# Performance work log

Hardware: AMD Instinct MI355X
Metric: run time of the kernel (lower is better)

## Reference

```python
import jax, jax.numpy as jnp
import numpy as np

N_NODES, N_EDGES, N_GRAPHS = 50000, 800000, 64
F_NODE, F_EDGE, F_GLOB, F_MSG, F_OUT, HID = 64, 64, 64, 64, 128, 32


def setup_inputs() -> dict:
    key = jax.random.key(0)
    ks = jax.random.split(key, 16)
    s = lambda fan_in: 1.0 / np.sqrt(fan_in)
    inp = {
        "x": jax.random.normal(ks[0], (N_NODES, F_NODE), dtype=jnp.float32),
        "edge_index": jax.random.randint(ks[1], (2, N_EDGES), 0, N_NODES),
        "edge_attr": jax.random.normal(ks[2], (N_EDGES, F_EDGE), dtype=jnp.float32),
        "u": jax.random.normal(ks[3], (N_GRAPHS, F_GLOB), dtype=jnp.float32),
        "batch": jnp.sort(jax.random.randint(ks[4], (N_NODES,), 0, N_GRAPHS)),
        # node_mlp_1: Lin(2*F_NODE+F_EDGE, 32) -> ReLU -> Lin(32, F_MSG) -> ReLU
        "W1": jax.random.normal(ks[5], (2 * F_NODE + F_EDGE, HID), dtype=jnp.float32) * s(2 * F_NODE + F_EDGE),
        "b1": jnp.zeros((HID,), jnp.float32),
        "W2": jax.random.normal(ks[6], (HID, F_MSG), dtype=jnp.float32) * s(HID),
        "b2": jnp.zeros((F_MSG,), jnp.float32),
        # node_mlp_2: Lin(2*F_MSG+F_NODE+F_GLOB, 32) -> ReLU -> Lin(32, F_OUT) -> ReLU
        "W3": jax.random.normal(ks[7], (2 * F_MSG + F_NODE + F_GLOB, HID), dtype=jnp.float32) * s(2 * F_MSG + F_NODE + F_GLOB),
        "b3": jnp.zeros((HID,), jnp.float32),
        "W4": jax.random.normal(ks[8], (HID, F_OUT), dtype=jnp.float32) * s(HID),
        "b4": jnp.zeros((F_OUT,), jnp.float32),
    }
    return inp


def reference(x, edge_index, edge_attr, u, batch, W1, b1, W2, b2, W3, b3, W4, b4):
    N = x.shape[0]
    row, col = edge_index[0], edge_index[1]
    # edge MLP (dropout off / eval mode)
    m = jnp.concatenate([x[row], x[col], edge_attr], axis=1)  # [E, 2F+Fe]
    m = jax.nn.relu(m @ W1 + b1)
    m = jax.nn.relu(m @ W2 + b2)  # [E, F_MSG]
    # scatter-mean and scatter-max onto destination nodes (col)
    cnt = jax.ops.segment_sum(jnp.ones((col.shape[0], 1), m.dtype), col, num_segments=N)  # [N,1]
    agg_mean = jax.ops.segment_sum(m, col, num_segments=N) / jnp.maximum(cnt, 1.0)
    agg_max = jax.ops.segment_max(m, col, num_segments=N)
    agg_max = jnp.where(cnt > 0, agg_max, 0.0)  # empty segments -> 0 (torch_scatter convention)
    # node MLP
    h = jnp.concatenate([x, agg_mean, agg_max, u[batch]], axis=1)
    h = jax.nn.relu(h @ W3 + b3)
    return jax.nn.relu(h @ W4 + b4)
```

## Files before the change

### kernel.cpp

```cpp
#include <hip/hip_runtime.h>
#include <hip/hip_bf16.h>
#include <stdint.h>

constexpr int FN   = 64;
constexpr int HIDN = 32;
constexpr int FMSG = 64;
constexpr int FOUT = 128;

using short8 = __attribute__((ext_vector_type(8))) short;
using f32x4  = __attribute__((ext_vector_type(4))) float;

union Frag { short8 v; uint32_t u[4]; };

__device__ __forceinline__ uint32_t packrn(float a, float b) {
    union { __hip_bfloat162 h; uint32_t u; } cv;
    cv.h = __float22bfloat162_rn(make_float2(a, b));
    return cv.u;
}
__device__ __forceinline__ float bf16_to_f(uint32_t h16) {
    return __uint_as_float(h16 << 16);
}

__device__ __forceinline__ int node_of(const int* __restrict__ offs, int N, int target) {
    int l = 0, r = N + 1;
    while (l + 1 < r) {
        const int m = (l + r) >> 1;
        if (offs[m] <= target) l = m; else r = m;
    }
    return l;
}

__global__ __launch_bounds__(256) void zero_cnt_kernel(int* __restrict__ cnt, int N)
{
    const int i = blockIdx.x * 256 + threadIdx.x;
    if (i < N) cnt[i] = 0;
}

__global__ __launch_bounds__(256) void hist_kernel(
    const int* __restrict__ ei, int* __restrict__ cnt, int* __restrict__ rank,
    int E)
{
    const int e4 = (blockIdx.x * 256 + threadIdx.x) * 4;
    if (e4 + 3 < E) {
        const int4 c = *reinterpret_cast<const int4*>(ei + E + e4);
        int4 r;
        r.x = atomicAdd(cnt + c.x, 1);
        r.y = atomicAdd(cnt + c.y, 1);
        r.z = atomicAdd(cnt + c.z, 1);
        r.w = atomicAdd(cnt + c.w, 1);
        *reinterpret_cast<int4*>(rank + e4) = r;
    } else {
        for (int e = e4; e < E; ++e) rank[e] = atomicAdd(cnt + ei[E + e], 1);
    }
}

__global__ __launch_bounds__(256) void prep_rest_kernel(
    const float* __restrict__ x, const float* __restrict__ u,
    const float* __restrict__ W1, const float* __restrict__ b1,
    const float* __restrict__ W2,
    const float* __restrict__ W3, const float* __restrict__ b3,
    const float* __restrict__ W4,
    float* __restrict__ Pa, float* __restrict__ Pb, float* __restrict__ Qc,
    float* __restrict__ Qu,
    uint32_t* __restrict__ PW1, uint32_t* __restrict__ PW2,
    uint32_t* __restrict__ PW3, uint32_t* __restrict__ PW4,
    uint4* __restrict__ zbase, size_t zquads,
    int N, int G, int BP, int BZ)
{
    const int b   = blockIdx.x;
    const int tid = threadIdx.x;

    if (b < BP) {
        const int n = b * 256 + tid;
        if (n >= N) return;
        float a[HIDN], bq[HIDN], c[HIDN];
#pragma unroll
        for (int j = 0; j < HIDN; ++j) { a[j] = b1[j]; bq[j] = 0.0f; c[j] = b3[j]; }
        const float* xr = x + (size_t)n * FN;
        const float* WA = W1;
        const float* WB = W1 + FN * HIDN;
        const float* WX = W3;
#pragma unroll 2
        for (int k = 0; k < FN; k += 4) {
            const float4 v = *reinterpret_cast<const float4*>(xr + k);
            const float* wa = WA + k * HIDN;
            const float* wb = WB + k * HIDN;
            const float* wc = WX + k * HIDN;
#pragma unroll
            for (int j = 0; j < HIDN; ++j) {
                float aj = a[j], bj = bq[j], cj = c[j];
                aj = fmaf(v.x, wa[j], aj);            bj = fmaf(v.x, wb[j], bj);            cj = fmaf(v.x, wc[j], cj);
                aj = fmaf(v.y, wa[HIDN + j], aj);     bj = fmaf(v.y, wb[HIDN + j], bj);     cj = fmaf(v.y, wc[HIDN + j], cj);
                aj = fmaf(v.z, wa[2 * HIDN + j], aj); bj = fmaf(v.z, wb[2 * HIDN + j], bj); cj = fmaf(v.z, wc[2 * HIDN + j], cj);
                aj = fmaf(v.w, wa[3 * HIDN + j], aj); bj = fmaf(v.w, wb[3 * HIDN + j], bj); cj = fmaf(v.w, wc[3 * HIDN + j], cj);
                a[j] = aj; bq[j] = bj; c[j] = cj;
            }
        }
        float4* pa = reinterpret_cast<float4*>(Pa + (size_t)n * HIDN);
        float4* pb = reinterpret_cast<float4*>(Pb + (size_t)n * HIDN);
        float4* qc = reinterpret_cast<float4*>(Qc + (size_t)n * HIDN);
#pragma unroll
        for (int q = 0; q < HIDN / 4; ++q) {
            pa[q] = make_float4(a[4*q], a[4*q+1], a[4*q+2], a[4*q+3]);
            pb[q] = make_float4(bq[4*q], bq[4*q+1], bq[4*q+2], bq[4*q+3]);
            qc[q] = make_float4(c[4*q], c[4*q+1], c[4*q+2], c[4*q+3]);
        }
        return;
    }
    if (b == BP) {
        const float* WC = W1 + 2 * FN * HIDN;
        for (int i = tid; i < 1024; i += 256) {
            const int j = i >> 5, k2 = i & 31;
            PW1[i] = packrn(WC[(2 * k2) * HIDN + j], WC[(2 * k2 + 1) * HIDN + j]);
        }
        for (int i = tid; i < 1024; i += 256) {
            const int j = i >> 4, k2 = i & 15;
            PW2[i] = packrn(W2[(2 * k2) * FMSG + j], W2[(2 * k2 + 1) * FMSG + j]);
        }
        const float* W3m = W3 + 64 * HIDN;
        for (int i = tid; i < 2048; i += 256) {
            const int j = i >> 6, k2 = i & 63;
            PW3[i] = packrn(W3m[(2 * k2) * HIDN + j], W3m[(2 * k2 + 1) * HIDN + j]);
        }
        for (int i = tid; i < 2048; i += 256) {
            const int j = i >> 4, k2 = i & 15;
            PW4[i] = packrn(W4[(2 * k2) * FOUT + j], W4[(2 * k2 + 1) * FOUT + j]);
        }
        const float* W3u = W3 + 192 * HIDN;
        for (int i = tid; i < G * HIDN; i += 256) {
            const int g = i >> 5, j = i & 31;
            const float* ur = u + (size_t)g * FN;
            float acc = 0.0f;
#pragma unroll 8
            for (int k = 0; k < FN; ++k) acc = fmaf(ur[k], W3u[k * HIDN + j], acc);
            Qu[i] = acc;
        }
        return;
    }
    const size_t stride = (size_t)BZ * 256;
    const uint4 z = make_uint4(0u, 0u, 0u, 0u);
    for (size_t i = (size_t)(b - BP - 1) * 256 + tid; i < zquads; i += stride)
        zbase[i] = z;
}

__global__ __launch_bounds__(256) void scanA_kernel(
    const int* __restrict__ cnt, int* __restrict__ part, int N)
{
    __shared__ int red[256];
    const int tid  = threadIdx.x;
    const int base = blockIdx.x * 2048 + tid * 8;
    int s = 0;
    if (base + 8 <= N) {
        const int4 a = *reinterpret_cast<const int4*>(cnt + base);
        const int4 b = *reinterpret_cast<const int4*>(cnt + base + 4);
        s = a.x + a.y + a.z + a.w + b.x + b.y + b.z + b.w;
    } else {
        for (int i = base; i < min(base + 8, N); ++i) s += cnt[i];
    }
    red[tid] = s;
    __syncthreads();
    for (int d = 128; d > 0; d >>= 1) {
        if (tid < d) red[tid] += red[tid + d];
        __syncthreads();
    }
    if (tid == 0) part[blockIdx.x] = red[0];
}

__global__ __launch_bounds__(64) void scanB_kernel(
    const int* __restrict__ part, int* __restrict__ partx,
    int* __restrict__ offs, int NB, int N)
{
    if (threadIdx.x == 0) {
        int run = 0;
        for (int i = 0; i < NB; ++i) { partx[i] = run; run += part[i]; }
        offs[N] = run;
    }
}

__global__ __launch_bounds__(256) void scanC_kernel(
    const int* __restrict__ cnt, const int* __restrict__ partx,
    int* __restrict__ offs, int N)
{
    __shared__ int sb[256];
    const int tid  = threadIdx.x;
    const int base = blockIdx.x * 2048 + tid * 8;
    int v[8];
    int tsum = 0;
#pragma unroll
    for (int q = 0; q < 8; ++q) {
        const int i = base + q;
        v[q] = (i < N) ? cnt[i] : 0;
        tsum += v[q];
    }
    sb[tid] = tsum;
    __syncthreads();
    for (int d = 1; d < 256; d <<= 1) {
        const int t = (tid >= d) ? sb[tid - d] : 0;
        __syncthreads();
        sb[tid] += t;
        __syncthreads();
    }
    int run = partx[blockIdx.x] + sb[tid] - tsum;
#pragma unroll
    for (int q = 0; q < 8; ++q) {
        const int i = base + q;
        if (i < N) offs[i] = run;
        run += v[q];
    }
}

__global__ __launch_bounds__(256) void scatter_ntile_kernel(
    const int* __restrict__ ei, const int* __restrict__ offs,
    const int* __restrict__ rank, int4* __restrict__ re4,
    int2* __restrict__ ntile, int E, int N, int NT, int SB)
{
    const int tid = threadIdx.x;
    if ((int)blockIdx.x < SB) {
        const int e = blockIdx.x * 256 + tid;
        if (e >= E) return;
        const int row = ei[e];
        const int col = ei[E + e];
        const int pos = offs[col] + rank[e];
        re4[pos] = make_int4(row, col, e, 0);
    } else {
        const int t = ((int)blockIdx.x - SB) * 256 + tid;
        if (t >= NT) return;
        const int a = node_of(offs, N, t * 64);
        const int b = node_of(offs, N, min(t * 64 + 63, E - 1));
        ntile[t] = make_int2(a, b);
    }
}

__global__ __launch_bounds__(128) void fused_edge_mfma(
    const float* __restrict__ ea,
    const uint32_t* __restrict__ PW1, const uint32_t* __restrict__ PW2,
    const float* __restrict__ b2,
    const float* __restrict__ Pa, const float* __restrict__ Pb,
    const int4* __restrict__ re4, const int* __restrict__ offs,
    const int2* __restrict__ ntile,
    float* __restrict__ agg_sum, int* __restrict__ agg_maxb,
    int N, int E, int NT)
{
    __shared__ uint32_t smem_all[2 * 64 * 34];
    const int w    = threadIdx.x >> 6;
    const int t    = blockIdx.x * 2 + w;
    if (t >= NT) return;
    uint32_t* smem = smem_all + w * (64 * 34);
    const int lane = threadIdx.x & 63;
    const int l15  = lane & 15;
    const int l4   = lane >> 4;
    const int e0   = t * 64;
    const int e1   = min(e0 + 64, E);
    const int2 nrange = ntile[t];

    const int p = e0 + lane;
    const int4 rce = re4[min(p, E - 1)];
    {
        const float2* pa = reinterpret_cast<const float2*>(Pa + (size_t)rce.x * HIDN);
        const float2* pb = reinterpret_cast<const float2*>(Pb + (size_t)rce.y * HIDN);
        float2* dst = reinterpret_cast<float2*>(&smem[lane * 34]);
#pragma unroll
        for (int q = 0; q < 16; ++q) {
            const float2 a = pa[q], b = pb[q];
            dst[q] = make_float2(a.x + b.x, a.y + b.y);
        }
    }

    Frag B1[2][2];
#pragma unroll
    for (int nt = 0; nt < 2; ++nt)
#pragma unroll
        for (int ks = 0; ks < 2; ++ks) {
            const uint4 q = *reinterpret_cast<const uint4*>(
                &PW1[(nt * 16 + l15) * 32 + ks * 16 + l4 * 4]);
            B1[nt][ks].u[0] = q.x; B1[nt][ks].u[1] = q.y;
            B1[nt][ks].u[2] = q.z; B1[nt][ks].u[3] = q.w;
        }
    Frag B2f[4];
#pragma unroll
    for (int nt = 0; nt < 4; ++nt) {
        const uint4 q = *reinterpret_cast<const uint4*>(
            &PW2[(nt * 16 + l15) * 16 + l4 * 4]);
        B2f[nt].u[0] = q.x; B2f[nt].u[1] = q.y;
        B2f[nt].u[2] = q.z; B2f[nt].u[3] = q.w;
    }

    Frag A1[4][2];
#pragma unroll
    for (int mt = 0; mt < 4; ++mt) {
        const int eix = __shfl(rce.z, mt * 16 + l15, 64);
        const float* rp = ea + (size_t)eix * FN;
#pragma unroll
        for (int ks = 0; ks < 2; ++ks) {
            const float4* gp = reinterpret_cast<const float4*>(rp + ks * 32 + l4 * 8);
            const float4 f0 = gp[0], f1 = gp[1];
            A1[mt][ks].u[0] = packrn(f0.x, f0.y);
            A1[mt][ks].u[1] = packrn(f0.z, f0.w);
            A1[mt][ks].u[2] = packrn(f1.x, f1.y);
            A1[mt][ks].u[3] = packrn(f1.z, f1.w);
        }
    }

    f32x4 acc1[4][2];
    const float* Pl = reinterpret_cast<const float*>(smem);
#pragma unroll
    for (int mt = 0; mt < 4; ++mt)
#pragma unroll
        for (int nt = 0; nt < 2; ++nt)
#pragma unroll
            for (int r = 0; r < 4; ++r) {
                const int et = mt * 16 + l4 * 4 + r;
                acc1[mt][nt][r] = Pl[et * 34 + nt * 16 + l15];
            }
#pragma unroll
    for (int mt = 0; mt < 4; ++mt)
#pragma unroll
        for (int nt = 0; nt < 2; ++nt)
#pragma unroll
            for (int ks = 0; ks < 2; ++ks)
                acc1[mt][nt] = __builtin_amdgcn_mfma_f32_16x16x32_bf16(
                    A1[mt][ks].v, B1[nt][ks].v, acc1[mt][nt], 0, 0, 0);

    float* Hl = reinterpret_cast<float*>(smem);
#pragma unroll
    for (int mt = 0; mt < 4; ++mt)
#pragma unroll
        for (int nt = 0; nt < 2; ++nt)
#pragma unroll
            for (int r = 0; r < 4; ++r) {
                const int et = mt * 16 + l4 * 4 + r;
                Hl[et * 34 + nt * 16 + l15] = fmaxf(acc1[mt][nt][r], 0.0f);
            }

    Frag A2[4];
#pragma unroll
    for (int mt = 0; mt < 4; ++mt) {
        const float* hb = &Hl[(mt * 16 + l15) * 34 + l4 * 8];
        const float2 g0 = *reinterpret_cast<const float2*>(hb + 0);
        const float2 g1 = *reinterpret_cast<const float2*>(hb + 2);
        const float2 g2 = *reinterpret_cast<const float2*>(hb + 4);
        const float2 g3 = *reinterpret_cast<const float2*>(hb + 6);
        A2[mt].u[0] = packrn(g0.x, g0.y);
        A2[mt].u[1] = packrn(g1.x, g1.y);
        A2[mt].u[2] = packrn(g2.x, g2.y);
        A2[mt].u[3] = packrn(g3.x, g3.y);
    }

#pragma unroll
    for (int nt = 0; nt < 4; ++nt) {
        const float b2v = b2[nt * 16 + l15];
        f32x4 a2c[4];
#pragma unroll
        for (int mt = 0; mt < 4; ++mt) {
            a2c[mt] = (f32x4){0.f, 0.f, 0.f, 0.f};
            a2c[mt] = __builtin_amdgcn_mfma_f32_16x16x32_bf16(
                A2[mt].v, B2f[nt].v, a2c[mt], 0, 0, 0);
        }
        const int j = nt * 16 + l15;
#pragma unroll
        for (int mt = 0; mt < 4; ++mt)
#pragma unroll
            for (int rp2 = 0; rp2 < 2; ++rp2) {
                const int q2 = mt * 8 + l4 * 2 + rp2;
                const float v0 = fmaxf(a2c[mt][rp2 * 2]     + b2v, 0.0f);
                const float v1 = fmaxf(a2c[mt][rp2 * 2 + 1] + b2v, 0.0f);
                smem[q2 * 64 + (j ^ (((q2 >> 1) & 1) << 4))] = packrn(v0, v1);
            }
    }

    const int n0 = nrange.x, n1 = nrange.y;
    for (int n = n0; n <= n1; ++n) {
        const int s0 = offs[n], t0 = offs[n + 1];
        const int sl = max(s0, e0) - e0, tl = min(t0, e1) - e0;
        float sum = 0.0f, mx = 0.0f;
        int q = sl;
        if (q < tl && (q & 1)) {
            const int q2 = q >> 1;
            const uint32_t wv = smem[q2 * 64 + (lane ^ (((q2 >> 1) & 1) << 4))];
            const float v = bf16_to_f(wv >> 16);
            sum += v; mx = fmaxf(mx, v); ++q;
        }
        for (; q + 1 < tl; q += 2) {
            const int q2 = q >> 1;
            const uint32_t wv = smem[q2 * 64 + (lane ^ (((q2 >> 1) & 1) << 4))];
            const float v0 = bf16_to_f(wv & 0xffffu), v1 = bf16_to_f(wv >> 16);
            sum += v0 + v1; mx = fmaxf(mx, fmaxf(v0, v1));
        }
        if (q < tl) {
            const int q2 = q >> 1;
            const uint32_t wv = smem[q2 * 64 + (lane ^ (((q2 >> 1) & 1) << 4))];
            const float v = bf16_to_f(wv & 0xffffu);
            sum += v; mx = fmaxf(mx, v);
        }
        float* sp = agg_sum  + (size_t)n * FMSG + lane;
        int*   mp = agg_maxb + (size_t)n * FMSG + lane;
        if (s0 >= e0 && t0 <= e1) {
            *sp = sum;
            *mp = __float_as_int(mx);
        } else {
            unsafeAtomicAdd(sp, sum);
            atomicMax(mp, __float_as_int(mx));
        }
    }
}

__global__ __launch_bounds__(256) void node_mfma(
    const float* __restrict__ Qc, const float* __restrict__ Qu,
    const int*   __restrict__ batch,
    const uint32_t* __restrict__ PW3, const uint32_t* __restrict__ PW4,
    const float* __restrict__ b4,
    const float* __restrict__ agg_sum, const int* __restrict__ agg_maxb,
    const int*   __restrict__ offs,
    float* __restrict__ out, int N)
{
    __shared__ float Hl_all[4 * 32 * 34];
    const int w    = threadIdx.x >> 6;
    float* Hl      = Hl_all + w * (32 * 34);
    const int lane = threadIdx.x & 63;
    const int l15  = lane & 15;
    const int l4   = lane >> 4;
    const int n0   = blockIdx.x * 128 + w * 32;
    if (n0 >= N) return;

    f32x4 acc1[2][2];
#pragma unroll
    for (int mt = 0; mt < 2; ++mt)
#pragma unroll
        for (int r = 0; r < 4; ++r) {
            const int nc = min(n0 + mt * 16 + l4 * 4 + r, N - 1);
            const int g  = batch[nc];
#pragma unroll
            for (int nt = 0; nt < 2; ++nt)
                acc1[mt][nt][r] = Qc[(size_t)nc * HIDN + nt * 16 + l15]
                                + Qu[(size_t)g  * HIDN + nt * 16 + l15];
        }

    int   arn[2];
    float ainv[2];
#pragma unroll
    for (int mt = 0; mt < 2; ++mt) {
        arn[mt] = min(n0 + mt * 16 + l15, N - 1);
        const int deg = offs[arn[mt] + 1] - offs[arn[mt]];
        ainv[mt] = (deg > 0) ? 1.0f / (float)deg : 0.0f;
    }

    Frag B3[2][4];
#pragma unroll
    for (int nt = 0; nt < 2; ++nt)
#pragma unroll
        for (int ks = 0; ks < 4; ++ks) {
            const uint4 q = *reinterpret_cast<const uint4*>(
                &PW3[(nt * 16 + l15) * 64 + ks * 16 + l4 * 4]);
            B3[nt][ks].u[0] = q.x; B3[nt][ks].u[1] = q.y;
            B3[nt][ks].u[2] = q.z; B3[nt][ks].u[3] = q.w;
        }

#pragma unroll
    for (int ks = 0; ks < 4; ++ks) {
        Frag A[2];
        if (ks < 2) {
#pragma unroll
            for (int mt = 0; mt < 2; ++mt) {
                const float4* gp = reinterpret_cast<const float4*>(
                    agg_sum + (size_t)arn[mt] * FMSG + ks * 32 + l4 * 8);
                const float4 f0 = gp[0], f1 = gp[1];
                const float s = ainv[mt];
                A[mt].u[0] = packrn(f0.x * s, f0.y * s);
                A[mt].u[1] = packrn(f0.z * s, f0.w * s);
                A[mt].u[2] = packrn(f1.x * s, f1.y * s);
                A[mt].u[3] = packrn(f1.z * s, f1.w * s);
            }
        } else {
#pragma unroll
            for (int mt = 0; mt < 2; ++mt) {
                const uint4* gp = reinterpret_cast<const uint4*>(
                    agg_maxb + (size_t)arn[mt] * FMSG + (ks - 2) * 32 + l4 * 8);
                const uint4 u0 = gp[0], u1 = gp[1];
                A[mt].u[0] = packrn(__uint_as_float(u0.x), __uint_as_float(u0.y));
                A[mt].u[1] = packrn(__uint_as_float(u0.z), __uint_as_float(u0.w));
                A[mt].u[2] = packrn(__uint_as_float(u1.x), __uint_as_float(u1.y));
                A[mt].u[3] = packrn(__uint_as_float(u1.z), __uint_as_float(u1.w));
            }
        }
#pragma unroll
        for (int mt = 0; mt < 2; ++mt)
#pragma unroll
            for (int nt = 0; nt < 2; ++nt)
                acc1[mt][nt] = __builtin_amdgcn_mfma_f32_16x16x32_bf16(
                    A[mt].v, B3[nt][ks].v, acc1[mt][nt], 0, 0, 0);
    }

#pragma unroll
    for (int mt = 0; mt < 2; ++mt)
#pragma unroll
        for (int nt = 0; nt < 2; ++nt)
#pragma unroll
            for (int r = 0; r < 4; ++r) {
                const int rw = mt * 16 + l4 * 4 + r;
                Hl[rw * 34 + nt * 16 + l15] = fmaxf(acc1[mt][nt][r], 0.0f);
            }

    Frag A2[2];
#pragma unroll
    for (int mt = 0; mt < 2; ++mt) {
        const float* hb = &Hl[(mt * 16 + l15) * 34 + l4 * 8];
        const float2 g0 = *reinterpret_cast<const float2*>(hb + 0);
        const float2 g1 = *reinterpret_cast<const float2*>(hb + 2);
        const float2 g2 = *reinterpret_cast<const float2*>(hb + 4);
        const float2 g3 = *reinterpret_cast<const float2*>(hb + 6);
        A2[mt].u[0] = packrn(g0.x, g0.y);
        A2[mt].u[1] = packrn(g1.x, g1.y);
        A2[mt].u[2] = packrn(g2.x, g2.y);
        A2[mt].u[3] = packrn(g3.x, g3.y);
    }

#pragma unroll
    for (int nt = 0; nt < 8; ++nt) {
        Frag B4f;
        const uint4 q = *reinterpret_cast<const uint4*>(
            &PW4[(nt * 16 + l15) * 16 + l4 * 4]);
        B4f.u[0] = q.x; B4f.u[1] = q.y; B4f.u[2] = q.z; B4f.u[3] = q.w;
        const float b4v = b4[nt * 16 + l15];
        f32x4 tacc[2];
#pragma unroll
        for (int mt = 0; mt < 2; ++mt) {
            tacc[mt] = (f32x4){0.f, 0.f, 0.f, 0.f};
            tacc[mt] = __builtin_amdgcn_mfma_f32_16x16x32_bf16(
                A2[mt].v, B4f.v, tacc[mt], 0, 0, 0);
        }
#pragma unroll
        for (int mt = 0; mt < 2; ++mt)
#pragma unroll
            for (int r = 0; r < 4; ++r) {
                const int node = n0 + mt * 16 + l4 * 4 + r;
                if (node < N)
                    out[(size_t)node * FOUT + nt * 16 + l15] =
                        fmaxf(tacc[mt][r] + b4v, 0.0f);
            }
    }
}

extern "C" void kernel_launch(void* const* d_in, const int* in_sizes, int n_in,
                              void* d_out, int out_size, void* d_ws, size_t ws_size,
                              hipStream_t stream)
{
    const float* x     = (const float*)d_in[0];
    const int*   ei    = (const int*)  d_in[1];
    const float* ea    = (const float*)d_in[2];
    const float* u     = (const float*)d_in[3];
    const int*   batch = (const int*)  d_in[4];
    const float* W1    = (const float*)d_in[5];
    const float* b1    = (const float*)d_in[6];
    const float* W2    = (const float*)d_in[7];
    const float* b2    = (const float*)d_in[8];
    const float* W3    = (const float*)d_in[9];
    const float* b3    = (const float*)d_in[10];
    const float* W4    = (const float*)d_in[11];
    const float* b4    = (const float*)d_in[12];
    float* out = (float*)d_out;

    const int N = in_sizes[0] / FN;
    const int E = in_sizes[1] / 2;
    const int G = in_sizes[3] / FN;
    const int NT = (E + 63) / 64;

    char* wp = (char*)d_ws;
    auto take = [&](size_t bytes) -> void* {
        void* r = (void*)wp;
        wp += (bytes + 255) & ~(size_t)255;
        return r;
    };
    float*    agg_sum  = (float*)   take((size_t)N * FMSG * 4);
    int*      agg_maxb = (int*)     take((size_t)N * FMSG * 4);
    char*     zero_end = wp;
    int*      cnt      = (int*)     take((size_t)N * 4);
    int*      offs     = (int*)     take(((size_t)N + 1) * 4);
    int*      rank     = (int*)     take((size_t)E * 4);
    int4*     re4      = (int4*)    take((size_t)E * 16);
    int2*     ntile    = (int2*)    take((size_t)NT * 8);
    float*    Pa       = (float*)   take((size_t)N * HIDN * 4);
    float*    Pb       = (float*)   take((size_t)N * HIDN * 4);
    float*    Qc       = (float*)   take((size_t)N * HIDN * 4);
    float*    Qu       = (float*)   take((size_t)G * HIDN * 4);
    uint32_t* PW1      = (uint32_t*)take(1024 * 4);
    uint32_t* PW2      = (uint32_t*)take(1024 * 4);
    uint32_t* PW3      = (uint32_t*)take(2048 * 4);
    uint32_t* PW4      = (uint32_t*)take(2048 * 4);
    int*      part     = (int*)     take(64 * 4);
    int*      partx    = (int*)     take(64 * 4);

    const int BH = (E / 4 + 255) / 256;
    const int BP = (N + 255) / 256;
    const int BZ = 256;
    const int NB = (N + 2047) / 2048;
    const int SB = (E + 255) / 256;
    const int TB = (NT + 255) / 256;
    const size_t zquads = (size_t)(zero_end - (char*)agg_sum) / 16;

    zero_cnt_kernel<<<(N + 255) / 256, 256, 0, stream>>>(cnt, N);
    hist_kernel   <<<BH, 256, 0, stream>>>(ei, cnt, rank, E);
    prep_rest_kernel<<<BP + 1 + BZ, 256, 0, stream>>>(
        x, u, W1, b1, W2, W3, b3, W4,
        Pa, Pb, Qc, Qu, PW1, PW2, PW3, PW4,
        (uint4*)agg_sum, zquads, N, G, BP, BZ);
    scanA_kernel  <<<NB, 256, 0, stream>>>(cnt, part, N);
    scanB_kernel  <<<1, 64, 0, stream>>>(part, partx, offs, NB, N);
    scanC_kernel  <<<NB, 256, 0, stream>>>(cnt, partx, offs, N);
    scatter_ntile_kernel<<<SB + TB, 256, 0, stream>>>(
        ei, offs, rank, re4, ntile, E, N, NT, SB);
    fused_edge_mfma<<<(NT + 1) / 2, 128, 0, stream>>>(
        ea, PW1, PW2, b2, Pa, Pb, re4, offs, ntile, agg_sum, agg_maxb, N, E, NT);
    node_mfma     <<<(N + 127) / 128, 256, 0, stream>>>(
        Qc, Qu, batch, PW3, PW4, b4, agg_sum, agg_maxb, offs, out, N);
}
```

Before: 226.5 us.

## Split node precompute into LDS-staged kernel and simplify histogram to one edge per thread

The per-node projection (x·W1a, x·W1b, x·W3x) moves into its own kernel. Each wave first stages 64 rows of x into padded shared memory with coalesced float4 loads, instead of every thread reading its own row with strided accesses. The weight packing, Qu and zeroing work move to a separate tail kernel. The histogram kernel now handles one edge per thread rather than four via int4, which trades memory-level parallelism per thread for more threads. The change adds a kernel launch and cuts the per-block thread count of the node kernel to 128.

```diff
diff --git a/kernel.cpp b/kernel.cpp
--- a/kernel.cpp
+++ b/kernel.cpp
@@ -40,74 +40,85 @@
     const int* __restrict__ ei, int* __restrict__ cnt, int* __restrict__ rank,
     int E)
 {
-    const int e4 = (blockIdx.x * 256 + threadIdx.x) * 4;
-    if (e4 + 3 < E) {
-        const int4 c = *reinterpret_cast<const int4*>(ei + E + e4);
-        int4 r;
-        r.x = atomicAdd(cnt + c.x, 1);
-        r.y = atomicAdd(cnt + c.y, 1);
-        r.z = atomicAdd(cnt + c.z, 1);
-        r.w = atomicAdd(cnt + c.w, 1);
-        *reinterpret_cast<int4*>(rank + e4) = r;
-    } else {
-        for (int e = e4; e < E; ++e) rank[e] = atomicAdd(cnt + ei[E + e], 1);
-    }
-}
-
-__global__ __launch_bounds__(256) void prep_rest_kernel(
-    const float* __restrict__ x, const float* __restrict__ u,
+    const int e = blockIdx.x * 256 + threadIdx.x;
+    if (e < E) rank[e] = atomicAdd(cnt + ei[E + e], 1);
+}
+
+__global__ __launch_bounds__(128) void node_pre_kernel(
+    const float* __restrict__ x,
     const float* __restrict__ W1, const float* __restrict__ b1,
-    const float* __restrict__ W2,
     const float* __restrict__ W3, const float* __restrict__ b3,
-    const float* __restrict__ W4,
     float* __restrict__ Pa, float* __restrict__ Pb, float* __restrict__ Qc,
+    int N)
+{
+    __shared__ float xs_all[2 * 64 * 65];
+    const int w    = threadIdx.x >> 6;
+    const int lane = threadIdx.x & 63;
+    float* xs = xs_all + w * (64 * 65);
+    const int nbase = blockIdx.x * 128 + w * 64;
+    if (nbase >= N) return;
+
+#pragma unroll
+    for (int j = 0; j < 16; ++j) {
+        const int idx = j * 64 + lane;
+        const int row = idx >> 4, cq = idx & 15;
+        const int nr  = min(nbase + row, N - 1);
+        const float4 v = *reinterpret_cast<const float4*>(x + (size_t)nr * FN + cq * 4);
+        float* d = xs + row * 65 + cq * 4;
+        d[0] = v.x; d[1] = v.y; d[2] = v.z; d[3] = v.w;
+    }
+
+    const int n = nbase + lane;
+    if (n >= N) return;
+
+    float a[HIDN], bq[HIDN], c[HIDN];
+#pragma unroll
+    for (int j = 0; j < HIDN; ++j) { a[j] = b1[j]; bq[j] = 0.0f; c[j] = b3[j]; }
+    const float* xr = xs + lane * 65;
+    const float* WA = W1;
+    const float* WB = W1 + FN * HIDN;
+    const float* WX = W3;
+#pragma unroll 2
+    for (int k = 0; k < FN; k += 4) {
+        const float v0 = xr[k], v1 = xr[k + 1], v2 = xr[k + 2], v3 = xr[k + 3];
+        const float* wa = WA + k * HIDN;
+        const float* wb = WB + k * HIDN;
+        const float* wc = WX + k * HIDN;
+#pragma unroll
+        for (int j = 0; j < HIDN; ++j) {
+            float aj = a[j], bj = bq[j], cj = c[j];
+            aj = fmaf(v0, wa[j], aj);            bj = fmaf(v0, wb[j], bj);            cj = fmaf(v0, wc[j], cj);
+            aj = fmaf(v1, wa[HIDN + j], aj);     bj = fmaf(v1, wb[HIDN + j], bj);     cj = fmaf(v1, wc[HIDN + j], cj);
+            aj = fmaf(v2, wa[2 * HIDN + j], aj); bj = fmaf(v2, wb[2 * HIDN + j], bj); cj = fmaf(v2, wc[2 * HIDN + j], cj);
+            aj = fmaf(v3, wa[3 * HIDN + j], aj); bj = fmaf(v3, wb[3 * HIDN + j], bj); cj = fmaf(v3, wc[3 * HIDN + j], cj);
+            a[j] = aj; bq[j] = bj; c[j] = cj;
+        }
+    }
+    float4* pa = reinterpret_cast<float4*>(Pa + (size_t)n * HIDN);
+    float4* pb = reinterpret_cast<float4*>(Pb + (size_t)n * HIDN);
+    float4* qc = reinterpret_cast<float4*>(Qc + (size_t)n * HIDN);
+#pragma unroll
+    for (int q = 0; q < HIDN / 4; ++q) {
+        pa[q] = make_float4(a[4*q], a[4*q+1], a[4*q+2], a[4*q+3]);
+        pb[q] = make_float4(bq[4*q], bq[4*q+1], bq[4*q+2], bq[4*q+3]);
+        qc[q] = make_float4(c[4*q], c[4*q+1], c[4*q+2], c[4*q+3]);
+    }
+}
+
+__global__ __launch_bounds__(256) void prep_tail_kernel(
+    const float* __restrict__ u,
+    const float* __restrict__ W1, const float* __restrict__ W2,
+    const float* __restrict__ W3, const float* __restrict__ W4,
     float* __restrict__ Qu,
     uint32_t* __restrict__ PW1, uint32_t* __restrict__ PW2,
     uint32_t* __restrict__ PW3, uint32_t* __restrict__ PW4,
     uint4* __restrict__ zbase, size_t zquads,
-    int N, int G, int BP, int BZ)
+    int G, int BZ)
 {
     const int b   = blockIdx.x;
     const int tid = threadIdx.x;
 
-    if (b < BP) {
-        const int n = b * 256 + tid;
-        if (n >= N) return;
-        float a[HIDN], bq[HIDN], c[HIDN];
-#pragma unroll
-        for (int j = 0; j < HIDN; ++j) { a[j] = b1[j]; bq[j] = 0.0f; c[j] = b3[j]; }
-        const float* xr = x + (size_t)n * FN;
-        const float* WA = W1;
-        const float* WB = W1 + FN * HIDN;
-        const float* WX = W3;
-#pragma unroll 2
-        for (int k = 0; k < FN; k += 4) {
-            const float4 v = *reinterpret_cast<const float4*>(xr + k);
-            const float* wa = WA + k * HIDN;
-            const float* wb = WB + k * HIDN;
-            const float* wc = WX + k * HIDN;
-#pragma unroll
-            for (int j = 0; j < HIDN; ++j) {
-                float aj = a[j], bj = bq[j], cj = c[j];
-                aj = fmaf(v.x, wa[j], aj);            bj = fmaf(v.x, wb[j], bj);            cj = fmaf(v.x, wc[j], cj);
-                aj = fmaf(v.y, wa[HIDN + j], aj);     bj = fmaf(v.y, wb[HIDN + j], bj);     cj = fmaf(v.y, wc[HIDN + j], cj);
-                aj = fmaf(v.z, wa[2 * HIDN + j], aj); bj = fmaf(v.z, wb[2 * HIDN + j], bj); cj = fmaf(v.z, wc[2 * HIDN + j], cj);
-                aj = fmaf(v.w, wa[3 * HIDN + j], aj); bj = fmaf(v.w, wb[3 * HIDN + j], bj); cj = fmaf(v.w, wc[3 * HIDN + j], cj);
-                a[j] = aj; bq[j] = bj; c[j] = cj;
-            }
-        }
-        float4* pa = reinterpret_cast<float4*>(Pa + (size_t)n * HIDN);
-        float4* pb = reinterpret_cast<float4*>(Pb + (size_t)n * HIDN);
-        float4* qc = reinterpret_cast<float4*>(Qc + (size_t)n * HIDN);
-#pragma unroll
-        for (int q = 0; q < HIDN / 4; ++q) {
-            pa[q] = make_float4(a[4*q], a[4*q+1], a[4*q+2], a[4*q+3]);
-            pb[q] = make_float4(bq[4*q], bq[4*q+1], bq[4*q+2], bq[4*q+3]);
-            qc[q] = make_float4(c[4*q], c[4*q+1], c[4*q+2], c[4*q+3]);
-        }
-        return;
-    }
-    if (b == BP) {
+    if (b == 0) {
         const float* WC = W1 + 2 * FN * HIDN;
         for (int i = tid; i < 1024; i += 256) {
             const int j = i >> 5, k2 = i & 31;
@@ -139,7 +150,7 @@
     }
     const size_t stride = (size_t)BZ * 256;
     const uint4 z = make_uint4(0u, 0u, 0u, 0u);
-    for (size_t i = (size_t)(b - BP - 1) * 256 + tid; i < zquads; i += stride)
+    for (size_t i = (size_t)(b - 1) * 256 + tid; i < zquads; i += stride)
         zbase[i] = z;
 }
 
@@ -589,8 +600,6 @@
     int*      part     = (int*)     take(64 * 4);
     int*      partx    = (int*)     take(64 * 4);
 
-    const int BH = (E / 4 + 255) / 256;
-    const int BP = (N + 255) / 256;
     const int BZ = 256;
     const int NB = (N + 2047) / 2048;
     const int SB = (E + 255) / 256;
@@ -598,18 +607,19 @@
     const size_t zquads = (size_t)(zero_end - (char*)agg_sum) / 16;
 
     zero_cnt_kernel<<<(N + 255) / 256, 256, 0, stream>>>(cnt, N);
-    hist_kernel   <<<BH, 256, 0, stream>>>(ei, cnt, rank, E);
-    prep_rest_kernel<<<BP + 1 + BZ, 256, 0, stream>>>(
-        x, u, W1, b1, W2, W3, b3, W4,
-        Pa, Pb, Qc, Qu, PW1, PW2, PW3, PW4,
-        (uint4*)agg_sum, zquads, N, G, BP, BZ);
-    scanA_kernel  <<<NB, 256, 0, stream>>>(cnt, part, N);
-    scanB_kernel  <<<1, 64, 0, stream>>>(part, partx, offs, NB, N);
-    scanC_kernel  <<<NB, 256, 0, stream>>>(cnt, partx, offs, N);
+    hist_kernel    <<<(E + 255) / 256, 256, 0, stream>>>(ei, cnt, rank, E);
+    node_pre_kernel<<<(N + 127) / 128, 128, 0, stream>>>(
+        x, W1, b1, W3, b3, Pa, Pb, Qc, N);
+    prep_tail_kernel<<<1 + BZ, 256, 0, stream>>>(
+        u, W1, W2, W3, W4, Qu, PW1, PW2, PW3, PW4,
+        (uint4*)agg_sum, zquads, G, BZ);
+    scanA_kernel   <<<NB, 256, 0, stream>>>(cnt, part, N);
+    scanB_kernel   <<<1, 64, 0, stream>>>(part, partx, offs, NB, N);
+    scanC_kernel   <<<NB, 256, 0, stream>>>(cnt, partx, offs, N);
     scatter_ntile_kernel<<<SB + TB, 256, 0, stream>>>(
         ei, offs, rank, re4, ntile, E, N, NT, SB);
     fused_edge_mfma<<<(NT + 1) / 2, 128, 0, stream>>>(
         ea, PW1, PW2, b2, Pa, Pb, re4, offs, ntile, agg_sum, agg_maxb, N, E, NT);
-    node_mfma     <<<(N + 127) / 128, 256, 0, stream>>>(
+    node_mfma      <<<(N + 127) / 128, 256, 0, stream>>>(
         Qc, Qu, batch, PW3, PW4, b4, agg_sum, agg_maxb, offs, out, N);
 }
```

Result: slower. 246.1 us (+8.6%).
